# Optimization experiments

Hardware: AMD Instinct MI355X
Metric: run time of the kernel (lower is better)

Reference implementation:

```python
import jax, jax.numpy as jnp
import numpy as np

B, T = 512, 16384


def fir(u, b, n_k):
    # u: [B, T], b: [n_b]. x[t] = sum_k b[k] * u[t - n_k - k] (zero init conditions)
    Tlen = u.shape[1]
    out = jnp.zeros_like(u)
    for k in range(b.shape[0]):  # small fixed taps (3)
        d = n_k + k
        shifted = jnp.pad(u, ((0, 0), (d, 0)))[:, :Tlen] if d > 0 else u
        out = out + b[k] * shifted
    return out


def ar_filter(x, a):
    # y[t] = x[t] - sum_j a[j] * y[t-1-j], zero initial conditions. x: [B, T], a: [n_a]
    na = a.shape[0]
    carry0 = jnp.zeros((x.shape[0], na), x.dtype)

    def step(carry, xt):  # carry[:, j] = y[t-1-j]
        yt = xt - carry @ a
        carry = jnp.concatenate([yt[:, None], carry[:, :-1]], axis=1)
        return carry, yt

    _, ys = jax.lax.scan(step, carry0, x.T)  # scan over time: [T, B]
    return ys.T


def lfilter(u, b, a, n_k):
    return ar_filter(fir(u, b, n_k), a)


def whf(x):
    # y = -elu(-10/11 * x)
    return -jax.nn.elu((-10.0 / 11.0) * x)


def setup_inputs() -> dict:
    key = jax.random.key(0)
    u = jax.random.normal(key, (B, T, 1), dtype=jnp.float32)
    b1 = jnp.array([0.2323, -0.6494, 0.5902], dtype=jnp.float32)
    a1 = jnp.array([-1.2091, 0.2653, 0.1169], dtype=jnp.float32)
    b2 = jnp.array([0.0957, -0.1619, 0.1107], dtype=jnp.float32)
    a2 = jnp.array([-1.2303, -0.1718, 0.4465], dtype=jnp.float32)
    return {"u": u, "b1": b1, "a1": a1, "b2": b2, "a2": a2}


def reference(u, b1, a1, b2, a2):
    x = u[..., 0]                      # [B, T]
    y1_lin = lfilter(x, b1, a1, n_k=1)
    y1_nl = whf(y1_lin)
    y2_lin = lfilter(y1_nl, b2, a2, n_k=0)
    return y2_lin[..., None]           # [B, T, 1]
```

## Files before the change

kernel.cpp:

```cpp
#include <hip/hip_runtime.h>
#include <hip/hip_fp16.h>


constexpr int T_LEN = 16384;
constexpr int NTH   = 256;

__global__ __launch_bounds__(NTH, 2)
void whsys_kernel(const float* __restrict__ u,
                  const float* __restrict__ b1v, const float* __restrict__ a1v,
                  const float* __restrict__ b2v, const float* __restrict__ a2v,
                  float* __restrict__ out)
{
    __shared__ uint2  u4[16 * 256];
    __shared__ float4 o_st[256 * 8];
    __shared__ float4 d1s[NTH + 1];
    __shared__ float4 d2s[NTH + 2];
    __shared__ float2 vts[NTH + 1];

    const int c = threadIdx.x;
    const float* __restrict__ urow = u   + (size_t)blockIdx.x * T_LEN;
    float*       __restrict__ orow = out + (size_t)blockIdx.x * T_LEN;

    const float b10=b1v[0], b11=b1v[1], b12=b1v[2];
    const float a10=a1v[0], a11=a1v[1], a12=a1v[2];
    const float b20=b2v[0], b21=b2v[1], b22=b2v[2];
    const float a20=a2v[0], a21=a2v[1], a22=a2v[2];

    #pragma unroll
    for (int q = 0; q < 16; ++q) {
        const int t0 = q * 1024 + c * 4;
        const float4 v = *reinterpret_cast<const float4*>(urow + t0);
        const int k  = q * 16 + (c >> 4);
        const int m4 = c & 15;
        const __half2 h01 = __floats2half2_rn(v.x, v.y);
        const __half2 h23 = __floats2half2_rn(v.z, v.w);
        uint2 pk;
        pk.x = __builtin_bit_cast(unsigned int, h01);
        pk.y = __builtin_bit_cast(unsigned int, h23);
        u4[m4 * 256 + (k ^ m4)] = pk;
    }
    if (c == 0) { d1s[0] = make_float4(0,0,0,0); vts[0] = make_float2(0,0); }
    if (c < 2)  { d2s[c] = make_float4(0,0,0,0); }

    float A[9] = {-a20, -a21, -a22,  1.f, 0.f, 0.f,  0.f, 1.f, 0.f};
    #pragma unroll
    for (int it = 0; it < 6; ++it) {
        float Bm[9];
        #pragma unroll
        for (int i = 0; i < 3; ++i)
            #pragma unroll
            for (int j = 0; j < 3; ++j)
                Bm[i*3+j] = fmaf(A[i*3+0], A[0+j],
                             fmaf(A[i*3+1], A[3+j], A[i*3+2] * A[6+j]));
        #pragma unroll
        for (int i = 0; i < 9; ++i) A[i] = Bm[i];
    }
    __syncthreads();

    auto unpack = [](uint2 pk) -> float4 {
        const __half2 h01 = __builtin_bit_cast(__half2, pk.x);
        const __half2 h23 = __builtin_bit_cast(__half2, pk.y);
        return make_float4(__half2float(h01.x), __half2float(h01.y),
                           __half2float(h23.x), __half2float(h23.y));
    };

    float y1v[64];
    {
        const int kc = (c > 0) ? c - 1 : 0;
        const float4 ut = unpack(u4[15 * 256 + (kc ^ 15)]);
        float u_m1 = (c > 0) ? ut.w : 0.f;
        float u_m2 = (c > 0) ? ut.z : 0.f;
        float u_m3 = (c > 0) ? ut.y : 0.f;
        #pragma unroll
        for (int g = 0; g < 16; ++g) {
            const float4 uu = unpack(u4[g * 256 + (c ^ g)]);
            const float us[4] = {uu.x, uu.y, uu.z, uu.w};
            #pragma unroll
            for (int e = 0; e < 4; ++e) {
                const int j = g * 4 + e;
                const float x = fmaf(b12, u_m3, fmaf(b11, u_m2, b10 * u_m1));
                const float ym1 = (j >= 1) ? y1v[j-1] : 0.f;
                const float ym2 = (j >= 2) ? y1v[j-2] : 0.f;
                const float ym3 = (j >= 3) ? y1v[j-3] : 0.f;
                y1v[j] = fmaf(-a10, ym1, fmaf(-a11, ym2, fmaf(-a12, ym3, x)));
                u_m3 = u_m2; u_m2 = u_m1; u_m1 = us[e];
            }
        }
    }
    d1s[c + 1] = make_float4(y1v[63], y1v[62], y1v[61], 0.f);
    __syncthreads();

    {
        const float4 E1 = d1s[c];
        float h1 = E1.x, h2 = E1.y, h3 = E1.z;
        #pragma unroll
        for (int j = 0; j < 64; ++j) {
            const float h = fmaf(-a10, h1, fmaf(-a11, h2, -a12 * h3));
            h3 = h2; h2 = h1; h1 = h;
            const float y1 = y1v[j] + h;
            const float t1 = 0.9090909090909091f * y1;
            const float bb = 1.f - __expf(-t1);
            y1v[j] = __builtin_amdgcn_fmed3f(t1, bb, 0.f);
        }
    }
    vts[c + 1] = make_float2(y1v[62], y1v[63]);
    __syncthreads();

    float y2a[64];
    {
        const float2 vt = vts[c];
        float v_m1 = vt.y, v_m2 = vt.x;
        #pragma unroll
        for (int j = 0; j < 64; ++j) {
            const float vj = y1v[j];
            const float x = fmaf(b22, v_m2, fmaf(b21, v_m1, b20 * vj));
            const float ym1 = (j >= 1) ? y2a[j-1] : 0.f;
            const float ym2 = (j >= 2) ? y2a[j-2] : 0.f;
            const float ym3 = (j >= 3) ? y2a[j-3] : 0.f;
            y2a[j] = fmaf(-a20, ym1, fmaf(-a21, ym2, fmaf(-a22, ym3, x)));
            v_m2 = v_m1; v_m1 = vj;
        }
    }
    d2s[c + 2] = make_float4(y2a[63], y2a[62], y2a[61], 0.f);
    __syncthreads();

    {
        const float4 Dm1 = d2s[c + 1];
        const float4 Dm2 = d2s[c];
        float g1 = fmaf(A[0], Dm2.x, fmaf(A[1], Dm2.y, fmaf(A[2], Dm2.z, Dm1.x)));
        float g2 = fmaf(A[3], Dm2.x, fmaf(A[4], Dm2.y, fmaf(A[5], Dm2.z, Dm1.y)));
        float g3 = fmaf(A[6], Dm2.x, fmaf(A[7], Dm2.y, fmaf(A[8], Dm2.z, Dm1.z)));
        #pragma unroll
        for (int p = 0; p < 2; ++p) {
            #pragma unroll
            for (int g8 = 0; g8 < 8; ++g8) {
                float ob[4];
                #pragma unroll
                for (int e = 0; e < 4; ++e) {
                    const int j = p * 32 + g8 * 4 + e;
                    const float h = fmaf(-a20, g1, fmaf(-a21, g2, -a22 * g3));
                    g3 = g2; g2 = g1; g1 = h;
                    ob[e] = y2a[j] + h;
                }
                o_st[c * 8 + (g8 ^ (c & 7))] =
                    make_float4(ob[0], ob[1], ob[2], ob[3]);
            }
            __syncthreads();
            #pragma unroll
            for (int i = 0; i < 8; ++i) {
                const int k = i * 32 + (c >> 3);
                const int e = c & 7;
                const float4 ov = o_st[k * 8 + (e ^ (k & 7))];
                *reinterpret_cast<float4*>(orow + k * 64 + p * 32 + e * 4) = ov;
            }
            __syncthreads();
        }
    }
}

extern "C" void kernel_launch(void* const* d_in, const int* in_sizes, int n_in,
                              void* d_out, int out_size, void* d_ws, size_t ws_size,
                              hipStream_t stream) {
    const float* u  = (const float*)d_in[0];
    const float* b1 = (const float*)d_in[1];
    const float* a1 = (const float*)d_in[2];
    const float* b2 = (const float*)d_in[3];
    const float* a2 = (const float*)d_in[4];
    float* out = (float*)d_out;

    const int B = in_sizes[0] / T_LEN;
    whsys_kernel<<<B, NTH, 0, stream>>>(u, b1, a1, b2, a2, out);
}
```

Baseline: 21.37 us.

## Split each row into 512 chunks of 32 and fuse WHF with second filter pass

```diff
diff --git a/kernel.cpp b/kernel.cpp
--- a/kernel.cpp
+++ b/kernel.cpp
@@ -3,19 +3,21 @@
 
 
 constexpr int T_LEN = 16384;
-constexpr int NTH   = 256;
+constexpr int NTH   = 512;
+constexpr int NCH   = 512;
 
-__global__ __launch_bounds__(NTH, 2)
+__global__ __launch_bounds__(NTH, 4)
 void whsys_kernel(const float* __restrict__ u,
                   const float* __restrict__ b1v, const float* __restrict__ a1v,
                   const float* __restrict__ b2v, const float* __restrict__ a2v,
                   float* __restrict__ out)
 {
-    __shared__ uint2  u4[16 * 256];
-    __shared__ float4 o_st[256 * 8];
-    __shared__ float4 d1s[NTH + 1];
-    __shared__ float4 d2s[NTH + 2];
-    __shared__ float2 vts[NTH + 1];
+    __shared__ __align__(16) unsigned char smem[32768];
+    uint2*  u4   = reinterpret_cast<uint2*>(smem);
+    float4* o_st = reinterpret_cast<float4*>(smem);
+    __shared__ float4 d1s[NCH + 2];
+    __shared__ float4 d2s[NCH + 3];
+    __shared__ float2 vts[NCH + 1];
 
     const int c = threadIdx.x;
     const float* __restrict__ urow = u   + (size_t)blockIdx.x * T_LEN;
@@ -27,34 +29,43 @@
     const float a20=a2v[0], a21=a2v[1], a22=a2v[2];
 
     #pragma unroll
-    for (int q = 0; q < 16; ++q) {
-        const int t0 = q * 1024 + c * 4;
+    for (int q = 0; q < 8; ++q) {
+        const int t0 = q * 2048 + c * 4;
         const float4 v = *reinterpret_cast<const float4*>(urow + t0);
-        const int k  = q * 16 + (c >> 4);
-        const int m4 = c & 15;
+        const int k64 = q * 32 + (c >> 4);
+        const int m   = c & 15;
         const __half2 h01 = __floats2half2_rn(v.x, v.y);
         const __half2 h23 = __floats2half2_rn(v.z, v.w);
         uint2 pk;
         pk.x = __builtin_bit_cast(unsigned int, h01);
         pk.y = __builtin_bit_cast(unsigned int, h23);
-        u4[m4 * 256 + (k ^ m4)] = pk;
+        u4[m * 256 + (k64 ^ m)] = pk;
     }
-    if (c == 0) { d1s[0] = make_float4(0,0,0,0); vts[0] = make_float2(0,0); }
-    if (c < 2)  { d2s[c] = make_float4(0,0,0,0); }
+    if (c < 2) d1s[c] = make_float4(0,0,0,0);
+    if (c < 3) d2s[c] = make_float4(0,0,0,0);
+    if (c == 0) vts[0] = make_float2(0,0);
 
-    float A[9] = {-a20, -a21, -a22,  1.f, 0.f, 0.f,  0.f, 1.f, 0.f};
+    float A1[9] = {-a10,-a11,-a12, 1.f,0.f,0.f, 0.f,1.f,0.f};
+    float A2[9] = {-a20,-a21,-a22, 1.f,0.f,0.f, 0.f,1.f,0.f};
+    float A2q[9];
     #pragma unroll
-    for (int it = 0; it < 6; ++it) {
-        float Bm[9];
+    for (int it = 0; it < 5; ++it) {
+        float B1[9], B2[9];
         #pragma unroll
         for (int i = 0; i < 3; ++i)
             #pragma unroll
-            for (int j = 0; j < 3; ++j)
-                Bm[i*3+j] = fmaf(A[i*3+0], A[0+j],
-                             fmaf(A[i*3+1], A[3+j], A[i*3+2] * A[6+j]));
+            for (int j = 0; j < 3; ++j) {
+                B1[i*3+j] = fmaf(A1[i*3], A1[j], fmaf(A1[i*3+1], A1[3+j], A1[i*3+2]*A1[6+j]));
+                B2[i*3+j] = fmaf(A2[i*3], A2[j], fmaf(A2[i*3+1], A2[3+j], A2[i*3+2]*A2[6+j]));
+            }
         #pragma unroll
-        for (int i = 0; i < 9; ++i) A[i] = Bm[i];
+        for (int i = 0; i < 9; ++i) { A1[i] = B1[i]; A2[i] = B2[i]; }
     }
+    #pragma unroll
+    for (int i = 0; i < 3; ++i)
+        #pragma unroll
+        for (int j = 0; j < 3; ++j)
+            A2q[i*3+j] = fmaf(A2[i*3], A2[j], fmaf(A2[i*3+1], A2[3+j], A2[i*3+2]*A2[6+j]));
     __syncthreads();
 
     auto unpack = [](uint2 pk) -> float4 {
@@ -63,98 +74,99 @@
         return make_float4(__half2float(h01.x), __half2float(h01.y),
                            __half2float(h23.x), __half2float(h23.y));
     };
+    auto whf = [](float y) -> float {
+        const float t1 = 0.9090909090909091f * y;
+        const float e  = 1.f - __expf(-t1);
+        return __builtin_amdgcn_fmed3f(t1, e, 0.f);
+    };
 
-    float y1v[64];
+    float arr[32];
+
     {
-        const int kc = (c > 0) ? c - 1 : 0;
-        const float4 ut = unpack(u4[15 * 256 + (kc ^ 15)]);
-        float u_m1 = (c > 0) ? ut.w : 0.f;
-        float u_m2 = (c > 0) ? ut.z : 0.f;
-        float u_m3 = (c > 0) ? ut.y : 0.f;
+        float u_m1 = 0.f, u_m2 = 0.f, u_m3 = 0.f;
+        if (c > 0) {
+            const int km1 = (c - 1) >> 1;
+            const int mm1 = 8 * ((c - 1) & 1) + 7;
+            const float4 ut = unpack(u4[mm1 * 256 + (km1 ^ mm1)]);
+            u_m1 = ut.w; u_m2 = ut.z; u_m3 = ut.y;
+        }
+        float yr1 = 0.f, yr2 = 0.f, yr3 = 0.f;
         #pragma unroll
-        for (int g = 0; g < 16; ++g) {
-            const float4 uu = unpack(u4[g * 256 + (c ^ g)]);
+        for (int g = 0; g < 8; ++g) {
+            const int m  = 8 * (c & 1) + g;
+            const int kk = c >> 1;
+            const float4 uu = unpack(u4[m * 256 + (kk ^ m)]);
             const float us[4] = {uu.x, uu.y, uu.z, uu.w};
             #pragma unroll
             for (int e = 0; e < 4; ++e) {
-                const int j = g * 4 + e;
                 const float x = fmaf(b12, u_m3, fmaf(b11, u_m2, b10 * u_m1));
-                const float ym1 = (j >= 1) ? y1v[j-1] : 0.f;
-                const float ym2 = (j >= 2) ? y1v[j-2] : 0.f;
-                const float ym3 = (j >= 3) ? y1v[j-3] : 0.f;
-                y1v[j] = fmaf(-a10, ym1, fmaf(-a11, ym2, fmaf(-a12, ym3, x)));
+                const float y = fmaf(-a10, yr1, fmaf(-a11, yr2, fmaf(-a12, yr3, x)));
+                arr[g * 4 + e] = y;
                 u_m3 = u_m2; u_m2 = u_m1; u_m1 = us[e];
+                yr3 = yr2; yr2 = yr1; yr1 = y;
             }
         }
+        d1s[c + 2] = make_float4(yr1, yr2, yr3, 0.f);
+        vts[c + 1] = make_float2(whf(yr2), whf(yr1));
     }
-    d1s[c + 1] = make_float4(y1v[63], y1v[62], y1v[61], 0.f);
     __syncthreads();
 
     {
-        const float4 E1 = d1s[c];
-        float h1 = E1.x, h2 = E1.y, h3 = E1.z;
+        const float4 P = d1s[c + 1], Q = d1s[c];
+        float h1 = fmaf(A1[0], Q.x, fmaf(A1[1], Q.y, fmaf(A1[2], Q.z, P.x)));
+        float h2 = fmaf(A1[3], Q.x, fmaf(A1[4], Q.y, fmaf(A1[5], Q.z, P.y)));
+        float h3 = fmaf(A1[6], Q.x, fmaf(A1[7], Q.y, fmaf(A1[8], Q.z, P.z)));
+        const float2 vt = vts[c];
+        float v1r = vt.y, v2r = vt.x;
+        float z1 = 0.f, z2 = 0.f, z3 = 0.f;
         #pragma unroll
-        for (int j = 0; j < 64; ++j) {
-            const float h = fmaf(-a10, h1, fmaf(-a11, h2, -a12 * h3));
-            h3 = h2; h2 = h1; h1 = h;
-            const float y1 = y1v[j] + h;
-            const float t1 = 0.9090909090909091f * y1;
-            const float bb = 1.f - __expf(-t1);
-            y1v[j] = __builtin_amdgcn_fmed3f(t1, bb, 0.f);
+        for (int j = 0; j < 32; ++j) {
+            const float hn = fmaf(-a10, h1, fmaf(-a11, h2, -a12 * h3));
+            h3 = h2; h2 = h1; h1 = hn;
+            const float v = whf(arr[j] + hn);
+            const float x = fmaf(b22, v2r, fmaf(b21, v1r, b20 * v));
+            const float z = fmaf(-a20, z1, fmaf(-a21, z2, fmaf(-a22, z3, x)));
+            v2r = v1r; v1r = v;
+            z3 = z2; z2 = z1; z1 = z;
+            arr[j] = z;
         }
+        d2s[c + 3] = make_float4(z1, z2, z3, 0.f);
     }
-    vts[c + 1] = make_float2(y1v[62], y1v[63]);
-    __syncthreads();
-
-    float y2a[64];
-    {
-        const float2 vt = vts[c];
-        float v_m1 = vt.y, v_m2 = vt.x;
-        #pragma unroll
-        for (int j = 0; j < 64; ++j) {
-            const float vj = y1v[j];
-            const float x = fmaf(b22, v_m2, fmaf(b21, v_m1, b20 * vj));
-            const float ym1 = (j >= 1) ? y2a[j-1] : 0.f;
-            const float ym2 = (j >= 2) ? y2a[j-2] : 0.f;
-            const float ym3 = (j >= 3) ? y2a[j-3] : 0.f;
-            y2a[j] = fmaf(-a20, ym1, fmaf(-a21, ym2, fmaf(-a22, ym3, x)));
-            v_m2 = v_m1; v_m1 = vj;
-        }
-    }
-    d2s[c + 2] = make_float4(y2a[63], y2a[62], y2a[61], 0.f);
     __syncthreads();
 
     {
-        const float4 Dm1 = d2s[c + 1];
-        const float4 Dm2 = d2s[c];
-        float g1 = fmaf(A[0], Dm2.x, fmaf(A[1], Dm2.y, fmaf(A[2], Dm2.z, Dm1.x)));
-        float g2 = fmaf(A[3], Dm2.x, fmaf(A[4], Dm2.y, fmaf(A[5], Dm2.z, Dm1.y)));
-        float g3 = fmaf(A[6], Dm2.x, fmaf(A[7], Dm2.y, fmaf(A[8], Dm2.z, Dm1.z)));
+        const float4 R = d2s[c + 2], S = d2s[c + 1], Tt = d2s[c];
+        float g1 = fmaf(A2[0], S.x, fmaf(A2[1], S.y, fmaf(A2[2], S.z,
+                   fmaf(A2q[0], Tt.x, fmaf(A2q[1], Tt.y, fmaf(A2q[2], Tt.z, R.x))))));
+        float g2 = fmaf(A2[3], S.x, fmaf(A2[4], S.y, fmaf(A2[5], S.z,
+                   fmaf(A2q[3], Tt.x, fmaf(A2q[4], Tt.y, fmaf(A2q[5], Tt.z, R.y))))));
+        float g3 = fmaf(A2[6], S.x, fmaf(A2[7], S.y, fmaf(A2[8], S.z,
+                   fmaf(A2q[6], Tt.x, fmaf(A2q[7], Tt.y, fmaf(A2q[8], Tt.z, R.z))))));
         #pragma unroll
-        for (int p = 0; p < 2; ++p) {
+        for (int j = 0; j < 32; ++j) {
+            const float gn = fmaf(-a20, g1, fmaf(-a21, g2, -a22 * g3));
+            g3 = g2; g2 = g1; g1 = gn;
+            arr[j] += gn;
+        }
+    }
+
+    #pragma unroll
+    for (int p = 0; p < 2; ++p) {
+        if ((c >> 8) == p) {
             #pragma unroll
-            for (int g8 = 0; g8 < 8; ++g8) {
-                float ob[4];
-                #pragma unroll
-                for (int e = 0; e < 4; ++e) {
-                    const int j = p * 32 + g8 * 4 + e;
-                    const float h = fmaf(-a20, g1, fmaf(-a21, g2, -a22 * g3));
-                    g3 = g2; g2 = g1; g1 = h;
-                    ob[e] = y2a[j] + h;
-                }
-                o_st[c * 8 + (g8 ^ (c & 7))] =
-                    make_float4(ob[0], ob[1], ob[2], ob[3]);
-            }
-            __syncthreads();
-            #pragma unroll
-            for (int i = 0; i < 8; ++i) {
-                const int k = i * 32 + (c >> 3);
-                const int e = c & 7;
-                const float4 ov = o_st[k * 8 + (e ^ (k & 7))];
-                *reinterpret_cast<float4*>(orow + k * 64 + p * 32 + e * 4) = ov;
-            }
-            __syncthreads();
+            for (int q = 0; q < 8; ++q)
+                o_st[(c & 255) * 8 + (q ^ (c & 7))] =
+                    make_float4(arr[4*q], arr[4*q+1], arr[4*q+2], arr[4*q+3]);
         }
+        __syncthreads();
+        #pragma unroll
+        for (int s = 0; s < 4; ++s) {
+            const int f = s * 512 + c;
+            const int k = f >> 3, q = f & 7;
+            const float4 ov = o_st[k * 8 + (q ^ (k & 7))];
+            *reinterpret_cast<float4*>(orow + (p * 256 + k) * 32 + q * 4) = ov;
+        }
+        if (p == 0) __syncthreads();
     }
 }
 
```

After: 21.34 us. No clear change (-0.2%).
